# Performance work log

Measured on AMD Instinct MI355X. Metric: run time of the kernel, lower is better.

Reference implementation:

```python
import jax, jax.numpy as jnp
import numpy as np

N_NODES = 200000
N_FRAGS = 50000
N_EDGES = 400000
HDIM = 128
VOCAB = 800


def setup_inputs() -> dict:
    key = jax.random.key(0)
    ks = jax.random.split(key, 9)
    x = jax.random.normal(ks[0], (N_NODES, HDIM), dtype=jnp.float32)
    fragments = jax.random.uniform(ks[1], (N_FRAGS, VOCAB), dtype=jnp.float32)
    emb_table = jax.random.normal(ks[2], (VOCAB, HDIM), dtype=jnp.float32)
    W_f = jax.random.normal(ks[3], (HDIM, HDIM), dtype=jnp.float32) / np.sqrt(HDIM)
    b_f = jax.random.normal(ks[4], (HDIM,), dtype=jnp.float32) * 0.01
    W_s = jax.random.normal(ks[5], (2 * HDIM, HDIM), dtype=jnp.float32) / np.sqrt(2 * HDIM)
    b_s = jax.random.normal(ks[6], (HDIM,), dtype=jnp.float32) * 0.01
    row = jax.random.randint(ks[7], (N_EDGES,), 0, N_NODES, dtype=jnp.int32)
    col = jax.random.randint(ks[8], (N_EDGES,), 0, N_FRAGS, dtype=jnp.int32)
    return {"x": x, "fragments": fragments, "emb_table": emb_table,
            "W_f": W_f, "b_f": b_f, "W_s": W_s, "b_s": b_s,
            "row": row, "col": col}


def _scatter_mean(vals, idx, num_segments):
    s = jax.ops.segment_sum(vals, idx, num_segments=num_segments)
    cnt = jax.ops.segment_sum(jnp.ones((vals.shape[0], 1), vals.dtype), idx,
                              num_segments=num_segments)
    return s / jnp.maximum(cnt, 1.0)


def reference(x, fragments, emb_table, W_f, b_f, W_s, b_s, row, col):
    N, H = x.shape
    F = fragments.shape[0]
    # gather node feats along memberships, mean-pool per fragment: [F, H]
    substructure_x = _scatter_mean(x[row], col, F)
    # fragment type embedding branch
    frag_ids = jnp.argmax(fragments, axis=1)            # [F]
    fragments_emb = emb_table[frag_ids] @ W_f + b_f      # [F, H]
    substructure_x = jnp.concatenate([substructure_x, fragments_emb], axis=1)  # [F, 2H]
    fragment_emb = substructure_x @ W_s + b_s            # [F, H]
    # gather fragment embeddings back to memberships, mean-pool per node: [N, H]
    return _scatter_mean(fragment_emb[col], row, N)
```

## Files before the change

### kernel.cpp

```cpp
#include <hip/hip_runtime.h>

#define HDIM 128
#define VOCAB 800
#define FB 16
#define TILE 1024
#define TILE_N 512

#define ACCB(a, h) { \
    a.x += __uint_as_float(h.x << 16); \
    a.y += __uint_as_float(h.x & 0xffff0000u); \
    a.z += __uint_as_float(h.y << 16); \
    a.w += __uint_as_float(h.y & 0xffff0000u); }

static __device__ __forceinline__ unsigned short f2bf(float f) {
    unsigned int u = __float_as_uint(f);
    return (unsigned short)((u + 0x7fffu + ((u >> 16) & 1u)) >> 16);
}

__global__ void k_prep(const float* __restrict__ emb, const float* __restrict__ W_f,
                       const float* __restrict__ W_s, const float* __restrict__ b_f,
                       const float* __restrict__ b_s, float* __restrict__ E2,
                       float* __restrict__ bfs) {
    __shared__ float e[HDIM], t1[HDIM];
    int j = threadIdx.x;
    int v = blockIdx.x;
    if (v < VOCAB) {
        e[j] = emb[(size_t)v * HDIM + j];
        __syncthreads();
        float a = 0.f;
        for (int k = 0; k < HDIM; ++k)
            a = fmaf(e[k], W_f[k * HDIM + j], a);
        t1[j] = a;
        __syncthreads();
        float b = 0.f;
        for (int k = 0; k < HDIM; ++k)
            b = fmaf(t1[k], W_s[(HDIM + k) * HDIM + j], b);
        E2[(size_t)v * HDIM + j] = b;
    } else {
        e[j] = b_f[j];
        __syncthreads();
        float b = b_s[j];
        for (int k = 0; k < HDIM; ++k)
            b = fmaf(e[k], W_s[(HDIM + k) * HDIM + j], b);
        bfs[j] = b;
    }
}

__global__ void k_cvt(const float* __restrict__ x, unsigned short* __restrict__ xb,
                      const int* __restrict__ row, const int* __restrict__ col,
                      int* __restrict__ cntr, int* __restrict__ cntc) {
    int b = blockIdx.x, t = threadIdx.x;
    if (b < 12500) {
        size_t i = ((size_t)b * 256 + t) * 8;
        float4 v0 = *reinterpret_cast<const float4*>(x + i);
        float4 v1 = *reinterpret_cast<const float4*>(x + i + 4);
        uint4 o;
        o.x = (unsigned)f2bf(v0.x) | ((unsigned)f2bf(v0.y) << 16);
        o.y = (unsigned)f2bf(v0.z) | ((unsigned)f2bf(v0.w) << 16);
        o.z = (unsigned)f2bf(v1.x) | ((unsigned)f2bf(v1.y) << 16);
        o.w = (unsigned)f2bf(v1.z) | ((unsigned)f2bf(v1.w) << 16);
        *reinterpret_cast<uint4*>(xb + i) = o;
    } else {
        int i = (b - 12500) * 256 + t;
        if (i < 100000) {
            int4 r4 = reinterpret_cast<const int4*>(row)[i];
            int4 c4 = reinterpret_cast<const int4*>(col)[i];
            atomicAdd(&cntr[r4.x], 1); atomicAdd(&cntr[r4.y], 1);
            atomicAdd(&cntr[r4.z], 1); atomicAdd(&cntr[r4.w], 1);
            atomicAdd(&cntc[c4.x], 1); atomicAdd(&cntc[c4.y], 1);
            atomicAdd(&cntc[c4.z], 1); atomicAdd(&cntc[c4.w], 1);
        }
    }
}

__global__ void k_bsum2(const int* __restrict__ cntc, const int* __restrict__ cntr,
                        int* __restrict__ bsc, int* __restrict__ bsr, int NBC, int F, int N) {
    __shared__ int s[256];
    int t = threadIdx.x;
    const int* cnt;
    int* bsum;
    int bb, L;
    if ((int)blockIdx.x < NBC) { cnt = cntc; bsum = bsc; bb = blockIdx.x; L = F; }
    else                       { cnt = cntr; bsum = bsr; bb = blockIdx.x - NBC; L = N; }
    int i = bb * 256 + t;
    s[t] = (i < L) ? cnt[i] : 0;
    __syncthreads();
    for (int o = 128; o > 0; o >>= 1) {
        if (t < o) s[t] += s[t + o];
        __syncthreads();
    }
    if (t == 0) bsum[bb] = s[0];
}

__global__ void k_scan2(int* __restrict__ bsc, int* __restrict__ bsr, int nbc, int nbr) {
    __shared__ int s[1024];
    int* bsum = (blockIdx.x == 0) ? bsc : bsr;
    int nb    = (blockIdx.x == 0) ? nbc : nbr;
    int t = threadIdx.x;
    int v = (t < nb) ? bsum[t] : 0;
    s[t] = v;
    __syncthreads();
    for (int o = 1; o < 1024; o <<= 1) {
        int a = (t >= o) ? s[t - o] : 0;
        __syncthreads();
        s[t] += a;
        __syncthreads();
    }
    if (t < nb) bsum[t] = s[t] - v;
}

__global__ void k_base2(const int* __restrict__ cntc, const int* __restrict__ cntr,
                        const int* __restrict__ bsc, const int* __restrict__ bsr,
                        int* __restrict__ basec, int* __restrict__ baser,
                        int NBC, int F, int N) {
    __shared__ int s[256];
    int t = threadIdx.x;
    const int *cnt, *bsum;
    int* base;
    int bb, L;
    if ((int)blockIdx.x < NBC) { cnt = cntc; bsum = bsc; base = basec; bb = blockIdx.x; L = F; }
    else                       { cnt = cntr; bsum = bsr; base = baser; bb = blockIdx.x - NBC; L = N; }
    int i = bb * 256 + t;
    int v = (i < L) ? cnt[i] : 0;
    s[t] = v;
    __syncthreads();
    for (int o = 1; o < 256; o <<= 1) {
        int a = (t >= o) ? s[t - o] : 0;
        __syncthreads();
        s[t] += a;
        __syncthreads();
    }
    if (i < L) base[i] = bsum[bb] + s[t] - v;
}

__global__ void k_place(const int* __restrict__ row, const int* __restrict__ col,
                        const int* __restrict__ basec, const int* __restrict__ baser,
                        int* __restrict__ curc, int* __restrict__ curr,
                        int* __restrict__ payc, int* __restrict__ payr, int E) {
    int e = blockIdx.x * 256 + threadIdx.x;
    if (e >= E) return;
    int r = row[e], c = col[e];
    int pc = atomicAdd(&curc[c], 1);
    payc[basec[c] + pc] = r;
    int pr = atomicAdd(&curr[r], 1);
    payr[baser[r] + pr] = c;
}

__global__ __launch_bounds__(256) void k_frag(
        const unsigned short* __restrict__ xb, const float* __restrict__ frags,
        const int* __restrict__ basec, const int* __restrict__ cntc,
        const int* __restrict__ payc, const float* __restrict__ W_s,
        const float* __restrict__ E2, const float* __restrict__ bfs,
        unsigned short* __restrict__ fembb) {
    __shared__ float s[FB][HDIM];
    __shared__ int eidx[TILE];
    __shared__ int fidv[FB];
    int t = threadIdx.x;
    int g = t >> 5, l = t & 31;
    int fb = blockIdx.x * FB;
#pragma unroll
    for (int rep = 0; rep < 2; ++rep) {
        int f = rep * 8 + g;
        const float4* r = reinterpret_cast<const float4*>(frags + (size_t)(fb + f) * VOCAB);
        float best = -1e30f;
        int bidx = 0;
        for (int i = l; i < VOCAB / 4; i += 32) {
            float4 v = r[i];
            int bI = i * 4;
            if (v.x > best) { best = v.x; bidx = bI + 0; }
            if (v.y > best) { best = v.y; bidx = bI + 1; }
            if (v.z > best) { best = v.z; bidx = bI + 2; }
            if (v.w > best) { best = v.w; bidx = bI + 3; }
        }
        for (int off = 16; off > 0; off >>= 1) {
            float ov = __shfl_xor(best, off, 32);
            int   oi = __shfl_xor(bidx, off, 32);
            if (ov > best || (ov == best && oi < bidx)) { best = ov; bidx = oi; }
        }
        if (l == 0) fidv[f] = bidx;
    }
    int fi0 = fb + g, fi1 = fb + 8 + g;
    int st0 = basec[fi0], d0 = cntc[fi0];
    int st1 = basec[fi1], d1 = cntc[fi1];
    int p0 = basec[fb];
    int pend = basec[fb + FB - 1] + cntc[fb + FB - 1];
    const uint2* x2 = reinterpret_cast<const uint2*>(xb);
    float4 a0A = make_float4(0.f, 0.f, 0.f, 0.f), a0B = a0A, a1A = a0A, a1B = a0A;
    for (int tb = p0; tb < pend; tb += TILE) {
        int nload = min(TILE, pend - tb);
        for (int i = t; i < nload; i += 256) eidx[i] = payc[tb + i];
        __syncthreads();
        int lim = tb + nload;
        int lo0 = max(st0, tb) - tb, hi0 = min(st0 + d0, lim) - tb;
        int lo1 = max(st1, tb) - tb, hi1 = min(st1 + d1, lim) - tb;
        int m = max(hi0 - lo0, hi1 - lo1);
        for (int j = 0; j < m; j += 2) {
            if (lo0 + j < hi0)     { uint2 h = x2[(size_t)eidx[lo0 + j]     * 32 + l]; ACCB(a0A, h); }
            if (lo0 + j + 1 < hi0) { uint2 h = x2[(size_t)eidx[lo0 + j + 1] * 32 + l]; ACCB(a0B, h); }
            if (lo1 + j < hi1)     { uint2 h = x2[(size_t)eidx[lo1 + j]     * 32 + l]; ACCB(a1A, h); }
            if (lo1 + j + 1 < hi1) { uint2 h = x2[(size_t)eidx[lo1 + j + 1] * 32 + l]; ACCB(a1B, h); }
        }
        __syncthreads();
    }
    float inv0 = 1.0f / fmaxf((float)d0, 1.0f);
    float inv1 = 1.0f / fmaxf((float)d1, 1.0f);
    float4 r0, r1;
    r0.x = (a0A.x + a0B.x) * inv0; r0.y = (a0A.y + a0B.y) * inv0;
    r0.z = (a0A.z + a0B.z) * inv0; r0.w = (a0A.w + a0B.w) * inv0;
    r1.x = (a1A.x + a1B.x) * inv1; r1.y = (a1A.y + a1B.y) * inv1;
    r1.z = (a1A.z + a1B.z) * inv1; r1.w = (a1A.w + a1B.w) * inv1;
    *reinterpret_cast<float4*>(&s[g][l * 4]) = r0;
    *reinterpret_cast<float4*>(&s[8 + g][l * 4]) = r1;
    __syncthreads();
    int d = t & 127;
    int fh = t >> 7;
    float bv = bfs[d];
    float acc[8];
#pragma unroll
    for (int f = 0; f < 8; ++f)
        acc[f] = E2[(size_t)fidv[fh * 8 + f] * HDIM + d] + bv;
    for (int k = 0; k < HDIM; k += 4) {
        float w0 = W_s[(k + 0) * HDIM + d];
        float w1 = W_s[(k + 1) * HDIM + d];
        float w2 = W_s[(k + 2) * HDIM + d];
        float w3 = W_s[(k + 3) * HDIM + d];
#pragma unroll
        for (int f = 0; f < 8; ++f) {
            const float4 sv = *reinterpret_cast<const float4*>(&s[fh * 8 + f][k]);
            acc[f] = fmaf(sv.x, w0, acc[f]);
            acc[f] = fmaf(sv.y, w1, acc[f]);
            acc[f] = fmaf(sv.z, w2, acc[f]);
            acc[f] = fmaf(sv.w, w3, acc[f]);
        }
    }
#pragma unroll
    for (int f = 0; f < 8; ++f)
        fembb[(size_t)(fb + fh * 8 + f) * HDIM + d] = f2bf(acc[f]);
}

__global__ __launch_bounds__(256) void k_node(
        const unsigned short* __restrict__ fembb, const int* __restrict__ baser,
        const int* __restrict__ cntr, const int* __restrict__ payr,
        float* __restrict__ out, int N) {
    __shared__ int eidx[TILE_N];
    int t = threadIdx.x;
    int g = t >> 5, l = t & 31;
    int n0 = blockIdx.x * 64;
    int ng = n0 + g * 8;
    int p0 = baser[n0];
    int pend = baser[n0 + 63] + cntr[n0 + 63];
    const uint2* f2p = reinterpret_cast<const uint2*>(fembb);
    float4 a[8];
    int st_[8], dg_[8];
#pragma unroll
    for (int i = 0; i < 8; ++i) {
        st_[i] = baser[ng + i];
        dg_[i] = cntr[ng + i];
        a[i] = make_float4(0.f, 0.f, 0.f, 0.f);
    }
    for (int tb = p0; tb < pend; tb += TILE_N) {
        int nload = min(TILE_N, pend - tb);
        for (int i = t; i < nload; i += 256) eidx[i] = payr[tb + i];
        __syncthreads();
        int lim = tb + nload;
        int lo[8], hi[8];
        int m = 0;
#pragma unroll
        for (int i = 0; i < 8; ++i) {
            lo[i] = max(st_[i], tb) - tb;
            hi[i] = min(st_[i] + dg_[i], lim) - tb;
            m = max(m, hi[i] - lo[i]);
        }
        for (int j = 0; j < m; ++j) {
#pragma unroll
            for (int i = 0; i < 8; ++i) {
                if (lo[i] + j < hi[i]) {
                    uint2 h = f2p[(size_t)eidx[lo[i] + j] * 32 + l];
                    ACCB(a[i], h);
                }
            }
        }
        __syncthreads();
    }
    float4* o4 = reinterpret_cast<float4*>(out);
#pragma unroll
    for (int i = 0; i < 8; ++i) {
        float inv = 1.0f / fmaxf((float)dg_[i], 1.0f);
        float4 r;
        r.x = a[i].x * inv; r.y = a[i].y * inv;
        r.z = a[i].z * inv; r.w = a[i].w * inv;
        o4[(size_t)(ng + i) * 32 + l] = r;
    }
}

extern "C" void kernel_launch(void* const* d_in, const int* in_sizes, int n_in,
                              void* d_out, int out_size, void* d_ws, size_t ws_size,
                              hipStream_t stream) {
    const float* x         = (const float*)d_in[0];
    const float* fragments = (const float*)d_in[1];
    const float* emb_table = (const float*)d_in[2];
    const float* W_f       = (const float*)d_in[3];
    const float* b_f       = (const float*)d_in[4];
    const float* W_s       = (const float*)d_in[5];
    const float* b_s       = (const float*)d_in[6];
    const int*   row       = (const int*)d_in[7];
    const int*   col       = (const int*)d_in[8];
    float* out = (float*)d_out;

    const int N = 200000, F = 50000, E = 400000;
    const int NBC = (F + 255) / 256;
    const int NBR = (N + 255) / 256;

    unsigned short* xb = (unsigned short*)d_out;

    unsigned short* fembb = (unsigned short*)d_ws;
    int* cntc  = (int*)(fembb + (size_t)F * HDIM);
    int* cntr  = cntc + F;
    int* curc  = cntr + N;
    int* curr  = curc + F;
    int* basec = curr + N;
    int* baser = basec + F;
    int* bsc   = baser + N;
    int* bsr   = bsc + 1024;
    int* payc  = bsr + 1024;
    int* payr  = payc + E;
    float* E2  = (float*)(payr + E);
    float* bfs = E2 + VOCAB * HDIM;

    hipMemsetAsync(cntc, 0, (size_t)(2 * (F + N)) * sizeof(int), stream);

    k_prep<<<VOCAB + 1, HDIM, 0, stream>>>(emb_table, W_f, W_s, b_f, b_s, E2, bfs);
    k_cvt<<<12500 + 391, 256, 0, stream>>>(x, xb, row, col, cntr, cntc);
    k_bsum2<<<NBC + NBR, 256, 0, stream>>>(cntc, cntr, bsc, bsr, NBC, F, N);
    k_scan2<<<2, 1024, 0, stream>>>(bsc, bsr, NBC, NBR);
    k_base2<<<NBC + NBR, 256, 0, stream>>>(cntc, cntr, bsc, bsr, basec, baser, NBC, F, N);
    k_place<<<(E + 255) / 256, 256, 0, stream>>>(row, col, basec, baser, curc, curr,
                                                 payc, payr, E);
    k_frag<<<F / FB, 256, 0, stream>>>(xb, fragments, basec, cntc, payc, W_s, E2, bfs, fembb);
    k_node<<<N / 64, 256, 0, stream>>>(fembb, baser, cntr, payr, out, N);
}
```

Baseline: 282.2 us.

## Move fragment argmax into conversion kernel and reuse scan bases as placement cursors

After: 251.0 us. 11.1% less time.

```diff
diff --git a/kernel.cpp b/kernel.cpp
--- a/kernel.cpp
+++ b/kernel.cpp
@@ -3,8 +3,11 @@
 #define HDIM 128
 #define VOCAB 800
 #define FB 16
+#define NB 64
 #define TILE 1024
 #define TILE_N 512
+
+typedef float f4 __attribute__((ext_vector_type(4)));
 
 #define ACCB(a, h) { \
     a.x += __uint_as_float(h.x << 16); \
@@ -46,21 +49,32 @@
     }
 }
 
-__global__ void k_cvt(const float* __restrict__ x, unsigned short* __restrict__ xb,
+__global__ void k_amc(const float* __restrict__ frags, int* __restrict__ frag_id,
+                      const float* __restrict__ x, unsigned short* __restrict__ xb,
                       const int* __restrict__ row, const int* __restrict__ col,
                       int* __restrict__ cntr, int* __restrict__ cntc) {
     int b = blockIdx.x, t = threadIdx.x;
     if (b < 12500) {
-        size_t i = ((size_t)b * 256 + t) * 8;
-        float4 v0 = *reinterpret_cast<const float4*>(x + i);
-        float4 v1 = *reinterpret_cast<const float4*>(x + i + 4);
-        uint4 o;
-        o.x = (unsigned)f2bf(v0.x) | ((unsigned)f2bf(v0.y) << 16);
-        o.y = (unsigned)f2bf(v0.z) | ((unsigned)f2bf(v0.w) << 16);
-        o.z = (unsigned)f2bf(v1.x) | ((unsigned)f2bf(v1.y) << 16);
-        o.w = (unsigned)f2bf(v1.z) | ((unsigned)f2bf(v1.w) << 16);
-        *reinterpret_cast<uint4*>(xb + i) = o;
-    } else {
+        int wave = b * 4 + (t >> 6);
+        int lane = t & 63;
+        const f4* r = reinterpret_cast<const f4*>(frags + (size_t)wave * VOCAB);
+        float best = -1e30f;
+        int bidx = 0;
+        for (int i = lane; i < VOCAB / 4; i += 64) {
+            f4 v = __builtin_nontemporal_load(r + i);
+            int base = i * 4;
+            if (v.x > best) { best = v.x; bidx = base + 0; }
+            if (v.y > best) { best = v.y; bidx = base + 1; }
+            if (v.z > best) { best = v.z; bidx = base + 2; }
+            if (v.w > best) { best = v.w; bidx = base + 3; }
+        }
+        for (int off = 32; off > 0; off >>= 1) {
+            float ov = __shfl_xor(best, off, 64);
+            int   oi = __shfl_xor(bidx, off, 64);
+            if (ov > best || (ov == best && oi < bidx)) { best = ov; bidx = oi; }
+        }
+        if (lane == 0) frag_id[wave] = bidx;
+    } else if (b < 12891) {
         int i = (b - 12500) * 256 + t;
         if (i < 100000) {
             int4 r4 = reinterpret_cast<const int4*>(row)[i];
@@ -70,6 +84,17 @@
             atomicAdd(&cntc[c4.x], 1); atomicAdd(&cntc[c4.y], 1);
             atomicAdd(&cntc[c4.z], 1); atomicAdd(&cntc[c4.w], 1);
         }
+    } else {
+        size_t i = (size_t)(b - 12891) * 256 + t;
+        const f4* xp = reinterpret_cast<const f4*>(x);
+        f4 v0 = __builtin_nontemporal_load(xp + 2 * i);
+        f4 v1 = __builtin_nontemporal_load(xp + 2 * i + 1);
+        uint4 o;
+        o.x = (unsigned)f2bf(v0.x) | ((unsigned)f2bf(v0.y) << 16);
+        o.y = (unsigned)f2bf(v0.z) | ((unsigned)f2bf(v0.w) << 16);
+        o.z = (unsigned)f2bf(v1.x) | ((unsigned)f2bf(v1.y) << 16);
+        o.w = (unsigned)f2bf(v1.z) | ((unsigned)f2bf(v1.w) << 16);
+        *reinterpret_cast<uint4*>(xb + i * 8) = o;
     }
 }
 
@@ -134,56 +159,36 @@
 }
 
 __global__ void k_place(const int* __restrict__ row, const int* __restrict__ col,
-                        const int* __restrict__ basec, const int* __restrict__ baser,
-                        int* __restrict__ curc, int* __restrict__ curr,
+                        int* __restrict__ basec, int* __restrict__ baser,
                         int* __restrict__ payc, int* __restrict__ payr, int E) {
     int e = blockIdx.x * 256 + threadIdx.x;
     if (e >= E) return;
     int r = row[e], c = col[e];
-    int pc = atomicAdd(&curc[c], 1);
-    payc[basec[c] + pc] = r;
-    int pr = atomicAdd(&curr[r], 1);
-    payr[baser[r] + pr] = c;
+    int pc = atomicAdd(&basec[c], 1);
+    payc[pc] = r;
+    int pr = atomicAdd(&baser[r], 1);
+    payr[pr] = c;
 }
 
 __global__ __launch_bounds__(256) void k_frag(
-        const unsigned short* __restrict__ xb, const float* __restrict__ frags,
-        const int* __restrict__ basec, const int* __restrict__ cntc,
-        const int* __restrict__ payc, const float* __restrict__ W_s,
-        const float* __restrict__ E2, const float* __restrict__ bfs,
-        unsigned short* __restrict__ fembb) {
+        const unsigned short* __restrict__ xb, const int* __restrict__ basec,
+        const int* __restrict__ payc, const int* __restrict__ frag_id,
+        const float* __restrict__ W_s, const float* __restrict__ E2,
+        const float* __restrict__ bfs, unsigned short* __restrict__ fembb) {
     __shared__ float s[FB][HDIM];
     __shared__ int eidx[TILE];
-    __shared__ int fidv[FB];
+    __shared__ int cb[FB + 1];
     int t = threadIdx.x;
     int g = t >> 5, l = t & 31;
     int fb = blockIdx.x * FB;
-#pragma unroll
-    for (int rep = 0; rep < 2; ++rep) {
-        int f = rep * 8 + g;
-        const float4* r = reinterpret_cast<const float4*>(frags + (size_t)(fb + f) * VOCAB);
-        float best = -1e30f;
-        int bidx = 0;
-        for (int i = l; i < VOCAB / 4; i += 32) {
-            float4 v = r[i];
-            int bI = i * 4;
-            if (v.x > best) { best = v.x; bidx = bI + 0; }
-            if (v.y > best) { best = v.y; bidx = bI + 1; }
-            if (v.z > best) { best = v.z; bidx = bI + 2; }
-            if (v.w > best) { best = v.w; bidx = bI + 3; }
-        }
-        for (int off = 16; off > 0; off >>= 1) {
-            float ov = __shfl_xor(best, off, 32);
-            int   oi = __shfl_xor(bidx, off, 32);
-            if (ov > best || (ov == best && oi < bidx)) { best = ov; bidx = oi; }
-        }
-        if (l == 0) fidv[f] = bidx;
-    }
-    int fi0 = fb + g, fi1 = fb + 8 + g;
-    int st0 = basec[fi0], d0 = cntc[fi0];
-    int st1 = basec[fi1], d1 = cntc[fi1];
-    int p0 = basec[fb];
-    int pend = basec[fb + FB - 1] + cntc[fb + FB - 1];
+    if (t <= FB) {
+        int idx = fb + t - 1;
+        cb[t] = (idx < 0) ? 0 : basec[idx];
+    }
+    __syncthreads();
+    int st0 = cb[g],     d0 = cb[g + 1] - cb[g];
+    int st1 = cb[8 + g], d1 = cb[9 + g] - cb[8 + g];
+    int p0 = cb[0], pend = cb[FB];
     const uint2* x2 = reinterpret_cast<const uint2*>(xb);
     float4 a0A = make_float4(0.f, 0.f, 0.f, 0.f), a0B = a0A, a1A = a0A, a1B = a0A;
     for (int tb = p0; tb < pend; tb += TILE) {
@@ -218,7 +223,7 @@
     float acc[8];
 #pragma unroll
     for (int f = 0; f < 8; ++f)
-        acc[f] = E2[(size_t)fidv[fh * 8 + f] * HDIM + d] + bv;
+        acc[f] = E2[(size_t)frag_id[fb + fh * 8 + f] * HDIM + d] + bv;
     for (int k = 0; k < HDIM; k += 4) {
         float w0 = W_s[(k + 0) * HDIM + d];
         float w1 = W_s[(k + 1) * HDIM + d];
@@ -240,24 +245,27 @@
 
 __global__ __launch_bounds__(256) void k_node(
         const unsigned short* __restrict__ fembb, const int* __restrict__ baser,
-        const int* __restrict__ cntr, const int* __restrict__ payr,
-        float* __restrict__ out, int N) {
+        const int* __restrict__ payr, float* __restrict__ out, int N) {
     __shared__ int eidx[TILE_N];
+    __shared__ int cb[NB + 1];
     int t = threadIdx.x;
     int g = t >> 5, l = t & 31;
-    int n0 = blockIdx.x * 64;
-    int ng = n0 + g * 8;
-    int p0 = baser[n0];
-    int pend = baser[n0 + 63] + cntr[n0 + 63];
+    int n0 = blockIdx.x * NB;
+    if (t <= NB) {
+        int idx = n0 + t - 1;
+        cb[t] = (idx < 0) ? 0 : baser[idx];
+    }
+    __syncthreads();
+    int st_[8], dg_[8];
+    float4 a[8];
+#pragma unroll
+    for (int i = 0; i < 8; ++i) {
+        st_[i] = cb[g * 8 + i];
+        dg_[i] = cb[g * 8 + i + 1] - st_[i];
+        a[i] = make_float4(0.f, 0.f, 0.f, 0.f);
+    }
+    int p0 = cb[0], pend = cb[NB];
     const uint2* f2p = reinterpret_cast<const uint2*>(fembb);
-    float4 a[8];
-    int st_[8], dg_[8];
-#pragma unroll
-    for (int i = 0; i < 8; ++i) {
-        st_[i] = baser[ng + i];
-        dg_[i] = cntr[ng + i];
-        a[i] = make_float4(0.f, 0.f, 0.f, 0.f);
-    }
     for (int tb = p0; tb < pend; tb += TILE_N) {
         int nload = min(TILE_N, pend - tb);
         for (int i = t; i < nload; i += 256) eidx[i] = payr[tb + i];
@@ -282,14 +290,14 @@
         }
         __syncthreads();
     }
-    float4* o4 = reinterpret_cast<float4*>(out);
+    f4* o4 = reinterpret_cast<f4*>(out);
 #pragma unroll
     for (int i = 0; i < 8; ++i) {
         float inv = 1.0f / fmaxf((float)dg_[i], 1.0f);
-        float4 r;
-        r.x = a[i].x * inv; r.y = a[i].y * inv;
-        r.z = a[i].z * inv; r.w = a[i].w * inv;
-        o4[(size_t)(ng + i) * 32 + l] = r;
+        f4 v;
+        v.x = a[i].x * inv; v.y = a[i].y * inv;
+        v.z = a[i].z * inv; v.w = a[i].w * inv;
+        __builtin_nontemporal_store(v, o4 + (size_t)(n0 + g * 8 + i) * 32 + l);
     }
 }
 
@@ -314,28 +322,26 @@
     unsigned short* xb = (unsigned short*)d_out;
 
     unsigned short* fembb = (unsigned short*)d_ws;
-    int* cntc  = (int*)(fembb + (size_t)F * HDIM);
-    int* cntr  = cntc + F;
-    int* curc  = cntr + N;
-    int* curr  = curc + F;
-    int* basec = curr + N;
-    int* baser = basec + F;
-    int* bsc   = baser + N;
-    int* bsr   = bsc + 1024;
-    int* payc  = bsr + 1024;
-    int* payr  = payc + E;
-    float* E2  = (float*)(payr + E);
-    float* bfs = E2 + VOCAB * HDIM;
-
-    hipMemsetAsync(cntc, 0, (size_t)(2 * (F + N)) * sizeof(int), stream);
-
-    k_prep<<<VOCAB + 1, HDIM, 0, stream>>>(emb_table, W_f, W_s, b_f, b_s, E2, bfs);
-    k_cvt<<<12500 + 391, 256, 0, stream>>>(x, xb, row, col, cntr, cntc);
+    int* cntc    = (int*)(fembb + (size_t)F * HDIM);
+    int* cntr    = cntc + F;
+    int* basec   = cntr + N;
+    int* baser   = basec + F;
+    int* bsc     = baser + N;
+    int* bsr     = bsc + 1024;
+    int* payc    = bsr + 1024;
+    int* payr    = payc + E;
+    int* frag_id = payr + E;
+    float* E2    = (float*)(frag_id + F);
+    float* bfs   = E2 + VOCAB * HDIM;
+
+    hipMemsetAsync(cntc, 0, (size_t)(F + N) * sizeof(int), stream);
+
+    k_amc<<<12891 + 12500, 256, 0, stream>>>(fragments, frag_id, x, xb, row, col, cntr, cntc);
     k_bsum2<<<NBC + NBR, 256, 0, stream>>>(cntc, cntr, bsc, bsr, NBC, F, N);
     k_scan2<<<2, 1024, 0, stream>>>(bsc, bsr, NBC, NBR);
     k_base2<<<NBC + NBR, 256, 0, stream>>>(cntc, cntr, bsc, bsr, basec, baser, NBC, F, N);
-    k_place<<<(E + 255) / 256, 256, 0, stream>>>(row, col, basec, baser, curc, curr,
-                                                 payc, payr, E);
-    k_frag<<<F / FB, 256, 0, stream>>>(xb, fragments, basec, cntc, payc, W_s, E2, bfs, fembb);
-    k_node<<<N / 64, 256, 0, stream>>>(fembb, baser, cntr, payr, out, N);
-}
+    k_place<<<(E + 255) / 256, 256, 0, stream>>>(row, col, basec, baser, payc, payr, E);
+    k_prep<<<VOCAB + 1, HDIM, 0, stream>>>(emb_table, W_f, W_s, b_f, b_s, E2, bfs);
+    k_frag<<<F / FB, 256, 0, stream>>>(xb, basec, payc, frag_id, W_s, E2, bfs, fembb);
+    k_node<<<N / NB, 256, 0, stream>>>(fembb, baser, payr, out, N);
+}
```
